# Performance work log

Hardware: AMD Instinct MI355X
Metric: run time of the kernel (lower is better)

Reference implementation:

```python
import jax, jax.numpy as jnp
import numpy as np

V, D, S, B = 32000, 1024, 2048, 4
H = 4 * D


def _sinusoidal_pe(max_len, d):
    position = np.arange(max_len, dtype=np.float32)[:, None]
    div_term = np.exp(np.arange(0, d, 2, dtype=np.float32) * (-np.log(10000.0) / d))
    pe = np.zeros((max_len, d), dtype=np.float32)
    pe[:, 0::2] = np.sin(position * div_term)
    pe[:, 1::2] = np.cos(position * div_term)
    return jnp.asarray(pe)


def setup_inputs() -> dict:
    key = jax.random.key(0)
    ks = jax.random.split(key, 13)
    std = 1.0 / np.sqrt(D)
    stdh = 1.0 / np.sqrt(H)
    w = lambda k, shp, s: (jax.random.normal(k, shp, jnp.float32) * s)
    inp = {
        "tokens": jax.random.randint(ks[0], (B, S), 0, V),
        "emb": jax.random.normal(ks[1], (V, D), jnp.float32),
        "pe": _sinusoidal_pe(S, D),
        "l1_wk": w(ks[2], (D, D), std),
        "l1_wv": w(ks[3], (D, D), std),
        "l1_wo": w(ks[4], (D, D), std),
        "l1_w1": w(ks[5], (D, H), std),
        "l1_w2": w(ks[6], (H, D), stdh),
        "l2_wk": w(ks[7], (D, D), std),
        "l2_wv": w(ks[8], (D, D), std),
        "l2_wo": w(ks[9], (D, D), std),
        "l2_w1": w(ks[10], (D, H), std),
        "l2_w2": w(ks[11], (H, D), stdh),
        "w_out": w(ks[12], (D, V), std),
    }
    return inp


def _block(h, mask, wk, wv, wo, w1, w2):
    d = h.shape[-1]
    xq = h                      # W_q is identity
    xk = h @ wk                 # [B,S,D]
    xv = h @ wv
    scores = jnp.einsum("bsd,btd->bst", xq, xk) / np.sqrt(float(d)) + mask
    attn = jax.nn.softmax(scores, axis=-1)          # [B,S,S]
    h_attn = jnp.einsum("bst,btd->bsd", attn, xv) @ wo
    h_res = h + h_attn
    h_ffn = jnp.maximum(h_res @ w1, 0.0) @ w2
    return h_res + h_ffn


def reference(tokens, emb, pe, l1_wk, l1_wv, l1_wo, l1_w1, l1_w2,
              l2_wk, l2_wv, l2_wo, l2_w1, l2_w2, w_out):
    seq_len = tokens.shape[1]
    h = emb[tokens] + pe[None, :seq_len, :]
    # causal additive mask: -inf above diagonal
    mask = jnp.triu(jnp.full((seq_len, seq_len), -jnp.inf, jnp.float32), k=1)
    h = _block(h, mask, l1_wk, l1_wv, l1_wo, l1_w1, l1_w2)
    h = _block(h, mask, l2_wk, l2_wv, l2_wo, l2_w1, l2_w2)
    logits = h[:, -1, :] @ w_out  # [B, V]
    return logits
```

## Files before the change

### kernel.cpp

```cpp
#include <hip/hip_runtime.h>

#define S_LEN 2048
#define D_DIM 1024
#define H_DIM 4096
#define V_DIM 32000
#define B_SZ  4

typedef float  f32x4  __attribute__((ext_vector_type(4)));
typedef __bf16 bf16x8 __attribute__((ext_vector_type(8)));

__device__ __forceinline__ ushort f2bf(float f) {
    union { float f; unsigned u; } v; v.f = f;
    unsigned r = v.u + 0x7fffu + ((v.u >> 16) & 1u);
    return (ushort)(r >> 16);
}

__global__ void bt_wtranspose(const float* __restrict__ in, ushort* __restrict__ out,
                              int R, int C) {
    __shared__ ushort s[64][65];
    int r0 = blockIdx.y * 64, c0 = blockIdx.x * 64;
    int t = threadIdx.x;
    int lr = t >> 2, lc4 = (t & 3) * 16;
    const float* src = in + (size_t)(r0 + lr) * C + c0 + lc4;
#pragma unroll
    for (int j = 0; j < 4; ++j) {
        float4 v = ((const float4*)src)[j];
        s[lr][lc4 + 4 * j + 0] = f2bf(v.x);
        s[lr][lc4 + 4 * j + 1] = f2bf(v.y);
        s[lr][lc4 + 4 * j + 2] = f2bf(v.z);
        s[lr][lc4 + 4 * j + 3] = f2bf(v.w);
    }
    __syncthreads();
    int oc = t >> 2, orr = (t & 3) * 16;
    ushort tmp[16] __attribute__((aligned(16)));
#pragma unroll
    for (int j = 0; j < 16; ++j) tmp[j] = s[orr + j][oc];
    ushort* dst = out + (size_t)(c0 + oc) * R + r0 + orr;
    *(uint4*)dst        = *(uint4*)tmp;
    *(uint4*)(dst + 8)  = *(uint4*)(tmp + 8);
}

__global__ void bt_embed(const int* __restrict__ tokens, const float* __restrict__ emb,
                         const float* __restrict__ pe, float* __restrict__ h,
                         ushort* __restrict__ hbf) {
    int row = blockIdx.x;
    int s   = row & (S_LEN - 1);
    int tok = tokens[row];
    int t   = threadIdx.x;
    float4 v = ((const float4*)(emb + (size_t)tok * D_DIM))[t];
    float4 p = ((const float4*)(pe + (size_t)s * D_DIM))[t];
    v.x += p.x; v.y += p.y; v.z += p.z; v.w += p.w;
    ((float4*)(h + (size_t)row * D_DIM))[t] = v;
    uint2 pk;
    pk.x = (unsigned)f2bf(v.x) | ((unsigned)f2bf(v.y) << 16);
    pk.y = (unsigned)f2bf(v.z) | ((unsigned)f2bf(v.w) << 16);
    ((uint2*)(hbf + (size_t)row * D_DIM))[t] = pk;
}

#define EPI_F32  0
#define EPI_BF16 1
#define EPI_RELU 2
#define EPI_RES  3

#define VMWAIT(N) asm volatile("s_waitcnt vmcnt(%0)" :: "n"(N) : "memory")
#define SBAR()  __builtin_amdgcn_s_barrier()
#define SCHED() __builtin_amdgcn_sched_barrier(0)
#define AS1 __attribute__((address_space(1)))
#define AS3 __attribute__((address_space(3)))

template <int BM, int BN, int EPI, bool CSKIP, bool KLIM>
__global__ __launch_bounds__(512, 1)
void bt_gemm8(const ushort* __restrict__ A, const ushort* __restrict__ B,
              float* Cf, ushort* Cb, const float* __restrict__ Res,
              int lda, int ldb, int ldc, int K,
              size_t strideA, size_t strideB, size_t strideC) {
    constexpr int MR = BM / 32;
    constexpr int NR = BN / 64;
    constexpr int Ak = BM / 128;
    constexpr int Bk = BN / 128;

    __shared__ ushort lds[2][(BM + BN) * 64];

    const int bm = blockIdx.y, bn = blockIdx.x;
    if (CSKIP && bn * BN >= (bm + 1) * BM) return;

    const int tid  = threadIdx.x;
    const int lane = tid & 63;
    const int wid  = tid >> 6;
    const int wr   = wid >> 2, wc = wid & 3;
    const int r15  = lane & 15, r4 = lane >> 4;
    const int lr   = lane >> 2;
    const int lsl  = lane & 3;
    const int kswz = (r4 ^ ((r15 >> 1) & 3)) * 8;

    const ushort* Ab = A + strideA * blockIdx.z + (size_t)bm * BM * lda;
    const ushort* Bb = B + strideB * blockIdx.z + (size_t)bn * BN * ldb;

    int NT = K >> 6;
    if (KLIM) { int lim = (bm + 1) * (BM / 64); if (lim < NT) NT = lim; }

    f32x4 acc[MR][NR];
#pragma unroll
    for (int m = 0; m < MR; ++m)
#pragma unroll
        for (int n = 0; n < NR; ++n) acc[m][n] = (f32x4){0.f, 0.f, 0.f, 0.f};

#define STAGE(t, kh)                                                              \
    {                                                                             \
        _Pragma("unroll")                                                         \
        for (int j = 0; j < Ak; ++j) {                                            \
            int row = (wid + j * 8) * 16 + lr;                                    \
            int c   = (kh) * 4 + (lsl ^ ((lr >> 1) & 3));                         \
            __builtin_amdgcn_global_load_lds(                                     \
                (const AS1 void*)(Ab + (size_t)(t) * 64 + (size_t)row * lda + c * 8), \
                (AS3 void*)(&lds[(t) & 1][(kh) * BM * 32] + (wid + j * 8) * 512), 16, 0, 0); \
        }                                                                         \
        _Pragma("unroll")                                                         \
        for (int j = 0; j < Bk; ++j) {                                            \
            int row = (wid + j * 8) * 16 + lr;                                    \
            int c   = (kh) * 4 + (lsl ^ ((lr >> 1) & 3));                         \
            __builtin_amdgcn_global_load_lds(                                     \
                (const AS1 void*)(Bb + (size_t)(t) * 64 + (size_t)row * ldb + c * 8), \
                (AS3 void*)(&lds[(t) & 1][BM * 64 + (kh) * BN * 32] + (wid + j * 8) * 512), 16, 0, 0); \
        }                                                                         \
    }

#define PHASE_COMPUTE(t, kh)                                                      \
    {                                                                             \
        bf16x8 aq[MR], bq[NR];                                                    \
        _Pragma("unroll")                                                         \
        for (int m = 0; m < MR; ++m) {                                            \
            int row = wr * (BM / 2) + m * 16 + r15;                               \
            aq[m] = *(const bf16x8*)(&lds[(t) & 1][(kh) * BM * 32 + row * 32 + kswz]); \
        }                                                                         \
        _Pragma("unroll")                                                         \
        for (int n = 0; n < NR; ++n) {                                            \
            int col = wc * (BN / 4) + n * 16 + r15;                               \
            bq[n] = *(const bf16x8*)(&lds[(t) & 1][BM * 64 + (kh) * BN * 32 + col * 32 + kswz]); \
        }                                                                         \
        __builtin_amdgcn_s_setprio(1);                                            \
        _Pragma("unroll")                                                         \
        for (int m = 0; m < MR; ++m)                                              \
            _Pragma("unroll")                                                     \
            for (int n = 0; n < NR; ++n)                                          \
                acc[m][n] = __builtin_amdgcn_mfma_f32_16x16x32_bf16(aq[m], bq[n], acc[m][n], 0, 0, 0); \
        __builtin_amdgcn_s_setprio(0);                                            \
    }

    STAGE(0, 0); STAGE(0, 1);

    for (int t = 0; t < NT - 1; ++t) {
        VMWAIT(Ak + Bk); SBAR(); SCHED();
        STAGE(t + 1, 0);
        PHASE_COMPUTE(t, 0);
        SCHED();
        VMWAIT(Ak + Bk); SBAR(); SCHED();
        STAGE(t + 1, 1);
        PHASE_COMPUTE(t, 1);
        SCHED();
    }
    VMWAIT(Ak + Bk); SBAR(); SCHED();
    PHASE_COMPUTE(NT - 1, 0);
    SCHED();
    VMWAIT(0); SBAR(); SCHED();
    PHASE_COMPUTE(NT - 1, 1);

    size_t cz = strideC * blockIdx.z;
    const int rowb = bm * BM + wr * (BM / 2) + r4 * 4;
    const int colb = bn * BN + wc * (BN / 4) + r15;
#pragma unroll
    for (int m = 0; m < MR; ++m) {
#pragma unroll
        for (int r = 0; r < 4; ++r) {
            int row = rowb + m * 16 + r;
            size_t base = cz + (size_t)row * ldc + colb;
#pragma unroll
            for (int n = 0; n < NR; ++n) {
                float v = acc[m][n][r];
                size_t idx = base + n * 16;
                if (EPI == EPI_F32)       Cf[idx] = v;
                else if (EPI == EPI_BF16) Cb[idx] = f2bf(v);
                else if (EPI == EPI_RELU) Cb[idx] = f2bf(fmaxf(v, 0.f));
                else { float o = v + Res[idx]; Cf[idx] = o; Cb[idx] = f2bf(o); }
            }
        }
    }
#undef STAGE
#undef PHASE_COMPUTE
}

__device__ __forceinline__ float wred_max(float v) {
#pragma unroll
    for (int off = 32; off; off >>= 1) v = fmaxf(v, __shfl_xor(v, off));
    return v;
}
__device__ __forceinline__ float wred_sum(float v) {
#pragma unroll
    for (int off = 32; off; off >>= 1) v += __shfl_xor(v, off);
    return v;
}

__global__ void bt_softmax(const float* __restrict__ scores, ushort* __restrict__ probs) {
    int row = blockIdx.x;
    int s   = row & (S_LEN - 1);
    const float* src = scores + (size_t)row * S_LEN;
    ushort*      dst = probs  + (size_t)row * S_LEN;
    int tid = threadIdx.x;
    int nvalid = s + 1;

    float vals[8];
    float mx = -1e30f;
#pragma unroll
    for (int j = 0; j < 8; ++j) {
        int t = tid + j * 256;
        float v = (t < nvalid) ? src[t] * 0.03125f : -1e30f;
        vals[j] = v;
        mx = fmaxf(mx, v);
    }
    __shared__ float red[4], red2[4];
    mx = wred_max(mx);
    if ((tid & 63) == 0) red[tid >> 6] = mx;
    __syncthreads();
    mx = fmaxf(fmaxf(red[0], red[1]), fmaxf(red[2], red[3]));

    float sum = 0.f, ps[8];
#pragma unroll
    for (int j = 0; j < 8; ++j) {
        float p = exp2f((vals[j] - mx) * 1.44269504f);
        ps[j] = p; sum += p;
    }
    sum = wred_sum(sum);
    if ((tid & 63) == 0) red2[tid >> 6] = sum;
    __syncthreads();
    sum = red2[0] + red2[1] + red2[2] + red2[3];
    float inv = 1.0f / sum;
#pragma unroll
    for (int j = 0; j < 8; ++j) {
        int t = tid + j * 256;
        dst[t] = (t < nvalid) ? f2bf(ps[j] * inv) : (ushort)0;
    }
}

__global__ void bt_logits(const float* __restrict__ h, const float* __restrict__ wout,
                          float* __restrict__ out) {
    __shared__ float hl[4][128];
    int tid = threadIdx.x;
    int d0 = blockIdx.y * 128;
    if (tid < 128) {
#pragma unroll
        for (int b = 0; b < 4; ++b)
            hl[b][tid] = h[((size_t)b * S_LEN + (S_LEN - 1)) * D_DIM + d0 + tid];
    }
    __syncthreads();
    int v = blockIdx.x * 256 + tid;
    float a0 = 0, a1 = 0, a2 = 0, a3 = 0;
    for (int j = 0; j < 128; ++j) {
        float w = wout[(size_t)(d0 + j) * V_DIM + v];
        a0 += hl[0][j] * w; a1 += hl[1][j] * w;
        a2 += hl[2][j] * w; a3 += hl[3][j] * w;
    }
    atomicAdd(out + v, a0);
    atomicAdd(out + V_DIM + v, a1);
    atomicAdd(out + 2 * V_DIM + v, a2);
    atomicAdd(out + 3 * V_DIM + v, a3);
}

extern "C" void kernel_launch(void* const* d_in, const int* in_sizes, int n_in,
                              void* d_out, int out_size, void* d_ws, size_t ws_size,
                              hipStream_t stream) {
    const int*   tokens = (const int*)d_in[0];
    const float* emb    = (const float*)d_in[1];
    const float* pe     = (const float*)d_in[2];
    const float* wgt[10];
    for (int i = 0; i < 10; ++i) wgt[i] = (const float*)d_in[3 + i];
    const float* wout = (const float*)d_in[13];

    char* w = (char*)d_ws;
    size_t o = 0;
    auto take = [&](size_t sz) { char* p = w + o; o += (sz + 255) & ~(size_t)255; return p; };

    const size_t DD = (size_t)D_DIM * D_DIM * 2;
    const size_t DH = (size_t)D_DIM * H_DIM * 2;
    size_t wsz[10] = {DD, DD, DD, DH, DH, DD, DD, DD, DH, DH};
    ushort* wT[10];
    for (int i = 0; i < 10; ++i) wT[i] = (ushort*)take(wsz[i]);

    const size_t NROW = (size_t)B_SZ * S_LEN;
    float*  h0     = (float*)take(NROW * D_DIM * 4);
    float*  h1     = (float*)take(NROW * D_DIM * 4);
    ushort* hbf    = (ushort*)take(NROW * D_DIM * 2);
    ushort* hresbf = (ushort*)take(NROW * D_DIM * 2);
    ushort* xkbf   = (ushort*)take(NROW * D_DIM * 2);
    ushort* xvt    = (ushort*)take((size_t)D_DIM * NROW * 2);
    ushort* hattn  = (ushort*)take(NROW * D_DIM * 2);
    char*   G      = take((size_t)B_SZ * S_LEN * S_LEN * 4 + (size_t)B_SZ * S_LEN * S_LEN * 2);
    float*  scores = (float*)G;
    ushort* probs  = (ushort*)(G + (size_t)B_SZ * S_LEN * S_LEN * 4);
    ushort* tbf    = (ushort*)G;

    int wR[10] = {1024, 1024, 1024, 1024, 4096, 1024, 1024, 1024, 1024, 4096};
    int wC[10] = {1024, 1024, 1024, 4096, 1024, 1024, 1024, 1024, 4096, 1024};
    for (int i = 0; i < 10; ++i)
        bt_wtranspose<<<dim3(wC[i] / 64, wR[i] / 64), 256, 0, stream>>>(wgt[i], wT[i], wR[i], wC[i]);

    bt_embed<<<NROW, 256, 0, stream>>>(tokens, emb, pe, h0, hbf);

    auto layer = [&](ushort* wk, ushort* wv2, ushort* wo, ushort* w1, ushort* w2) {
        bt_gemm8<256, 128, EPI_BF16, false, false><<<dim3(8, 32, 1), 512, 0, stream>>>(
            hbf, wk, nullptr, xkbf, nullptr, D_DIM, D_DIM, D_DIM, D_DIM, 0, 0, 0);
        bt_gemm8<128, 256, EPI_BF16, false, false><<<dim3(32, 8, 1), 512, 0, stream>>>(
            wv2, hbf, nullptr, xvt, nullptr, D_DIM, D_DIM, (int)NROW, D_DIM, 0, 0, 0);
        bt_gemm8<256, 128, EPI_F32, true, false><<<dim3(16, 8, B_SZ), 512, 0, stream>>>(
            hbf, xkbf, scores, nullptr, nullptr, D_DIM, D_DIM, S_LEN, D_DIM,
            (size_t)S_LEN * D_DIM, (size_t)S_LEN * D_DIM, (size_t)S_LEN * S_LEN);
        bt_softmax<<<NROW, 256, 0, stream>>>(scores, probs);
        bt_gemm8<256, 128, EPI_BF16, false, true><<<dim3(8, 8, B_SZ), 512, 0, stream>>>(
            probs, xvt, nullptr, hattn, nullptr, S_LEN, (int)NROW, D_DIM, S_LEN,
            (size_t)S_LEN * S_LEN, (size_t)S_LEN, (size_t)S_LEN * D_DIM);
        bt_gemm8<256, 128, EPI_RES, false, false><<<dim3(8, 32, 1), 512, 0, stream>>>(
            hattn, wo, h1, hresbf, h0, D_DIM, D_DIM, D_DIM, D_DIM, 0, 0, 0);
        bt_gemm8<256, 256, EPI_RELU, false, false><<<dim3(16, 32, 1), 512, 0, stream>>>(
            hresbf, w1, nullptr, tbf, nullptr, D_DIM, D_DIM, H_DIM, D_DIM, 0, 0, 0);
        bt_gemm8<256, 128, EPI_RES, false, false><<<dim3(8, 32, 1), 512, 0, stream>>>(
            tbf, w2, h0, hbf, h1, H_DIM, H_DIM, D_DIM, H_DIM, 0, 0, 0);
    };
    layer(wT[0], wT[1], wT[2], wT[3], wT[4]);
    layer(wT[5], wT[6], wT[7], wT[8], wT[9]);

    hipMemsetAsync(d_out, 0, (size_t)B_SZ * V_DIM * sizeof(float), stream);
    bt_logits<<<dim3(V_DIM / 256, D_DIM / 128), 256, 0, stream>>>(h0, wout, (float*)d_out);
}
```

Baseline: 913.8 us.

## Deepen GEMM LDS pipeline to four half-stages and add XCD-aware tile swizzle

New measurement: 830.8 us. 9.1% less time.

```diff
diff --git a/kernel.cpp b/kernel.cpp
--- a/kernel.cpp
+++ b/kernel.cpp
@@ -68,7 +68,7 @@
 #define AS1 __attribute__((address_space(1)))
 #define AS3 __attribute__((address_space(3)))
 
-template <int BM, int BN, int EPI, bool CSKIP, bool KLIM>
+template <int BM, int BN, int EPI, bool CSKIP, bool KLIM, int SWZ>
 __global__ __launch_bounds__(512, 1)
 void bt_gemm8(const ushort* __restrict__ A, const ushort* __restrict__ B,
               float* Cf, ushort* Cb, const float* __restrict__ Res,
@@ -78,10 +78,28 @@
     constexpr int NR = BN / 64;
     constexpr int Ak = BM / 128;
     constexpr int Bk = BN / 128;
-
-    __shared__ ushort lds[2][(BM + BN) * 64];
-
-    const int bm = blockIdx.y, bn = blockIdx.x;
+    constexpr int G  = Ak + Bk;
+    constexpr int HS = (BM + BN) * 32;
+
+    __shared__ ushort lds[4][HS];
+
+    int bm, bn;
+    if (SWZ == 1) {
+        int gx = gridDim.x, gy = gridDim.y;
+        int id = blockIdx.y * gx + blockIdx.x;
+        int xcd = id & 7, slot = id >> 3;
+        int bandH = gy >> 3;
+        bm = xcd * bandH + (slot % bandH);
+        bn = slot / bandH;
+    } else if (SWZ == 2) {
+        int gx = gridDim.x;
+        int id = blockIdx.y * gx + blockIdx.x;
+        int xcd = id & 7, slot = id >> 3;
+        int bandW = gx >> 3;
+        bn = xcd * bandW + (slot % bandW);
+        bm = slot / bandW;
+    } else { bm = blockIdx.y; bn = blockIdx.x; }
+
     if (CSKIP && bn * BN >= (bm + 1) * BM) return;
 
     const int tid  = threadIdx.x;
@@ -105,38 +123,40 @@
 #pragma unroll
         for (int n = 0; n < NR; ++n) acc[m][n] = (f32x4){0.f, 0.f, 0.f, 0.f};
 
-#define STAGE(t, kh)                                                              \
+#define STAGE(hs)                                                                 \
     {                                                                             \
+        const int t_ = (hs) >> 1, b_ = (hs) & 3;                                  \
+        const int c_ = ((hs) & 1) * 4 + (lsl ^ ((lr >> 1) & 3));                  \
         _Pragma("unroll")                                                         \
         for (int j = 0; j < Ak; ++j) {                                            \
             int row = (wid + j * 8) * 16 + lr;                                    \
-            int c   = (kh) * 4 + (lsl ^ ((lr >> 1) & 3));                         \
             __builtin_amdgcn_global_load_lds(                                     \
-                (const AS1 void*)(Ab + (size_t)(t) * 64 + (size_t)row * lda + c * 8), \
-                (AS3 void*)(&lds[(t) & 1][(kh) * BM * 32] + (wid + j * 8) * 512), 16, 0, 0); \
+                (const AS1 void*)(Ab + (size_t)t_ * 64 + (size_t)row * lda + c_ * 8), \
+                (AS3 void*)(&lds[b_][0] + (wid + j * 8) * 512), 16, 0, 0);        \
         }                                                                         \
         _Pragma("unroll")                                                         \
         for (int j = 0; j < Bk; ++j) {                                            \
             int row = (wid + j * 8) * 16 + lr;                                    \
-            int c   = (kh) * 4 + (lsl ^ ((lr >> 1) & 3));                         \
-            __builtin_amdgcn_global_load_lds(                                     \
-                (const AS1 void*)(Bb + (size_t)(t) * 64 + (size_t)row * ldb + c * 8), \
-                (AS3 void*)(&lds[(t) & 1][BM * 64 + (kh) * BN * 32] + (wid + j * 8) * 512), 16, 0, 0); \
+            __builtin_amdgcn_global_lo\
+ad_lds(                                                                           \
+                (const AS1 void*)(Bb + (size_t)t_ * 64 + (size_t)row * ldb + c_ * 8), \
+                (AS3 void*)(&lds[b_][BM * 32] + (wid + j * 8) * 512), 16, 0, 0);  \
         }                                                                         \
     }
 
-#define PHASE_COMPUTE(t, kh)                                                      \
+#define PHASE_COMPUTE(hs)                                                         \
     {                                                                             \
+        const int b_ = (hs) & 3;                                                  \
         bf16x8 aq[MR], bq[NR];                                                    \
         _Pragma("unroll")                                                         \
         for (int m = 0; m < MR; ++m) {                                            \
             int row = wr * (BM / 2) + m * 16 + r15;                               \
-            aq[m] = *(const bf16x8*)(&lds[(t) & 1][(kh) * BM * 32 + row * 32 + kswz]); \
+            aq[m] = *(const bf16x8*)(&lds[b_][row * 32 + kswz]);                  \
         }                                                                         \
         _Pragma("unroll")                                                         \
         for (int n = 0; n < NR; ++n) {                                            \
             int col = wc * (BN / 4) + n * 16 + r15;                               \
-            bq[n] = *(const bf16x8*)(&lds[(t) & 1][BM * 64 + (kh) * BN * 32 + col * 32 + kswz]); \
+            bq[n] = *(const bf16x8*)(&lds[b_][BM * 32 + col * 32 + kswz]);        \
         }                                                                         \
         __builtin_amdgcn_s_setprio(1);                                            \
         _Pragma("unroll")                                                         \
@@ -147,23 +167,23 @@
         __builtin_amdgcn_s_setprio(0);                                            \
     }
 
-    STAGE(0, 0); STAGE(0, 1);
-
-    for (int t = 0; t < NT - 1; ++t) {
-        VMWAIT(Ak + Bk); SBAR(); SCHED();
-        STAGE(t + 1, 0);
-        PHASE_COMPUTE(t, 0);
+    STAGE(0); STAGE(1); STAGE(2);
+
+    const int NH2 = 2 * NT;
+    for (int hs = 0; hs < NH2 - 3; ++hs) {
+        VMWAIT(2 * G); SBAR(); SCHED();
+        STAGE(hs + 3);
+        PHASE_COMPUTE(hs);
         SCHED();
-        VMWAIT(Ak + Bk); SBAR(); SCHED();
-        STAGE(t + 1, 1);
-        PHASE_COMPUTE(t, 1);
-        SCHED();
-    }
-    VMWAIT(Ak + Bk); SBAR(); SCHED();
-    PHASE_COMPUTE(NT - 1, 0);
+    }
+    VMWAIT(2 * G); SBAR(); SCHED();
+    PHASE_COMPUTE(NH2 - 3);
+    SCHED();
+    VMWAIT(G); SBAR(); SCHED();
+    PHASE_COMPUTE(NH2 - 2);
     SCHED();
     VMWAIT(0); SBAR(); SCHED();
-    PHASE_COMPUTE(NT - 1, 1);
+    PHASE_COMPUTE(NH2 - 1);
 
     size_t cz = strideC * blockIdx.z;
     const int rowb = bm * BM + wr * (BM / 2) + r4 * 4;
@@ -306,22 +326,22 @@
     bt_embed<<<NROW, 256, 0, stream>>>(tokens, emb, pe, h0, hbf);
 
     auto layer = [&](ushort* wk, ushort* wv2, ushort* wo, ushort* w1, ushort* w2) {
-        bt_gemm8<256, 128, EPI_BF16, false, false><<<dim3(8, 32, 1), 512, 0, stream>>>(
+        bt_gemm8<256, 128, EPI_BF16, false, false, 1><<<dim3(8, 32, 1), 512, 0, stream>>>(
             hbf, wk, nullptr, xkbf, nullptr, D_DIM, D_DIM, D_DIM, D_DIM, 0, 0, 0);
-        bt_gemm8<128, 256, EPI_BF16, false, false><<<dim3(32, 8, 1), 512, 0, stream>>>(
+        bt_gemm8<128, 256, EPI_BF16, false, false, 2><<<dim3(32, 8, 1), 512, 0, stream>>>(
             wv2, hbf, nullptr, xvt, nullptr, D_DIM, D_DIM, (int)NROW, D_DIM, 0, 0, 0);
-        bt_gemm8<256, 128, EPI_F32, true, false><<<dim3(16, 8, B_SZ), 512, 0, stream>>>(
+        bt_gemm8<256, 128, EPI_F32, true, false, 0><<<dim3(16, 8, B_SZ), 512, 0, stream>>>(
             hbf, xkbf, scores, nullptr, nullptr, D_DIM, D_DIM, S_LEN, D_DIM,
             (size_t)S_LEN * D_DIM, (size_t)S_LEN * D_DIM, (size_t)S_LEN * S_LEN);
         bt_softmax<<<NROW, 256, 0, stream>>>(scores, probs);
-        bt_gemm8<256, 128, EPI_BF16, false, true><<<dim3(8, 8, B_SZ), 512, 0, stream>>>(
+        bt_gemm8<256, 128, EPI_BF16, false, true, 0><<<dim3(8, 8, B_SZ), 512, 0, stream>>>(
             probs, xvt, nullptr, hattn, nullptr, S_LEN, (int)NROW, D_DIM, S_LEN,
             (size_t)S_LEN * S_LEN, (size_t)S_LEN, (size_t)S_LEN * D_DIM);
-        bt_gemm8<256, 128, EPI_RES, false, false><<<dim3(8, 32, 1), 512, 0, stream>>>(
+        bt_gemm8<256, 128, EPI_RES, false, false, 1><<<dim3(8, 32, 1), 512, 0, stream>>>(
             hattn, wo, h1, hresbf, h0, D_DIM, D_DIM, D_DIM, D_DIM, 0, 0, 0);
-        bt_gemm8<256, 256, EPI_RELU, false, false><<<dim3(16, 32, 1), 512, 0, stream>>>(
+        bt_gemm8<256, 256, EPI_RELU, false, false, 1><<<dim3(16, 32, 1), 512, 0, stream>>>(
             hresbf, w1, nullptr, tbf, nullptr, D_DIM, D_DIM, H_DIM, D_DIM, 0, 0, 0);
-        bt_gemm8<256, 128, EPI_RES, false, false><<<dim3(8, 32, 1), 512, 0, stream>>>(
+        bt_gemm8<256, 128, EPI_RES, false, false, 1><<<dim3(8, 32, 1), 512, 0, stream>>>(
             tbf, w2, h0, hbf, h1, H_DIM, H_DIM, D_DIM, H_DIM, 0, 0, 0);
     };
     layer(wT[0], wT[1], wT[2], wT[3], wT[4]);
```
